# Kernel optimization log

Hardware: AMD Instinct MI355X
Metric: run time of the kernel (lower is better)

The kernel has to match this reference:

```python
import jax, jax.numpy as jnp
import numpy as np

# Dimensions (match input_specs / init_kwargs)
B, T, M, H, E, K = 4, 2048, 1024, 2048, 8, 2
CAP_FACTOR = 1.0  # tutel default capacity_factor
S = B * T
C = int(K * CAP_FACTOR * ((S + E - 1) // E))  # per-expert capacity (tutel Top-k gate)


def setup_inputs() -> dict:
    key = jax.random.key(0)
    ks = jax.random.split(key, 4)
    x = jax.random.normal(ks[0], (B, T, M), jnp.float32)
    wg = jax.random.normal(ks[1], (M, E), jnp.float32) / np.sqrt(M)
    w1 = jax.random.normal(ks[2], (E, M, H), jnp.float32) / np.sqrt(M)
    b1 = jnp.zeros((E, H), jnp.float32)
    w2 = jax.random.normal(ks[3], (E, H, M), jnp.float32) / np.sqrt(H)
    b2 = jnp.zeros((E, M), jnp.float32)
    return {"x": x, "wg": wg, "w1": w1, "b1": b1, "w2": w2, "b2": b2}


def reference(x, wg, w1, b1, w2, b2):
    xf = x.reshape(S, M)
    # ---- Top-k gate (fp32 gate) ----
    logits = xf.astype(jnp.float32) @ wg                 # [S, E]
    scores = jax.nn.softmax(logits, axis=-1)
    topv, topi = jax.lax.top_k(scores, K)                # [S, K]
    gates = topv / (jnp.sum(topv, axis=-1, keepdims=True) + 1e-9)  # normalized top-k gates

    # ---- Dispatch into [E, C, M] buffer with capacity-based token dropping ----
    buf = jnp.zeros((E, C, M), xf.dtype)
    offset = jnp.zeros((E,), jnp.int32)  # tokens already placed per expert (previous slots)
    pos_list, keep_list = [], []
    for j in range(K):  # small fixed loop over top-k slots
        e = topi[:, j]                                   # [S]
        m = jax.nn.one_hot(e, E, dtype=jnp.int32)        # [S, E]
        pos = jnp.sum(jnp.cumsum(m, axis=0) * m, axis=1) - 1 + offset[e]  # position within expert
        offset = offset + jnp.sum(m, axis=0)
        keep = pos < C                                   # drop tokens over capacity
        posc = jnp.minimum(pos, C - 1)
        buf = buf.at[e, posc].add(xf * keep[:, None].astype(xf.dtype))
        pos_list.append(posc)
        keep_list.append(keep)

    # ---- Grouped expert FFN: relu(x W1 + b1) W2 + b2 ----
    h = jax.nn.relu(jnp.einsum('ecm,emh->ech', buf, w1) + b1[:, None, :])  # [E, C, H]
    y = jnp.einsum('ech,ehm->ecm', h, w2) + b2[:, None, :]                 # [E, C, M]

    # ---- Combine with gate weights ----
    out = jnp.zeros_like(xf)
    for j in range(K):
        g = gates[:, j] * keep_list[j].astype(xf.dtype)
        out = out + g[:, None] * y[topi[:, j], pos_list[j]]

    out = out.reshape(B, T, M)
    # result = log_softmax(sum over model_dim, over token dim)
    return jax.nn.log_softmax(jnp.sum(out, axis=2), axis=1)   # [B, T]
```

## Files before the change

### kernel.cpp

```cpp
#include <hip/hip_runtime.h>
#include <hip/hip_bf16.h>
#include <cstdint>
#include <cstddef>

constexpr int Bb = 4;
constexpr int Tt = 2048;
constexpr int Mm = 1024;
constexpr int Hh = 2048;
constexpr int Ee = 8;
constexpr int Ss = Bb * Tt;
constexpr int Cc = 2048;

typedef __attribute__((ext_vector_type(4))) float f32x4;
typedef __attribute__((ext_vector_type(8))) short bf16x8;

__device__ inline void load_lds16(const void* g, void* l) {
    __builtin_amdgcn_global_load_lds(
        (const __attribute__((address_space(1))) unsigned int*)g,
        (__attribute__((address_space(3))) unsigned int*)l, 16, 0, 0);
}

__global__ __launch_bounds__(256) void k_prep(
    const float* __restrict__ w1, const float* __restrict__ w2, const float* __restrict__ b2,
    const float* __restrict__ x, const float* __restrict__ wg,
    __hip_bfloat16* __restrict__ w1t, float* __restrict__ w2sum, float* __restrict__ b2sum,
    int* __restrict__ esel, float* __restrict__ gates, __hip_bfloat16* __restrict__ xbf) {
    int bid = blockIdx.x;
    int t = threadIdx.x;
    if (bid < 4096) {
        __shared__ float tile[64][65];
        int e = bid >> 9, m0 = ((bid >> 5) & 15) * 64, h0 = (bid & 31) * 64;
        const float* src = w1 + (size_t)e * Mm * Hh;
        #pragma unroll
        for (int i = 0; i < 4; i++) {
            int idx = t + i * 256;
            int r = idx >> 4, c4 = idx & 15;
            float4 v = *(const float4*)(src + (size_t)(m0 + r) * Hh + h0 + c4 * 4);
            tile[r][c4 * 4 + 0] = v.x; tile[r][c4 * 4 + 1] = v.y;
            tile[r][c4 * 4 + 2] = v.z; tile[r][c4 * 4 + 3] = v.w;
        }
        __syncthreads();
        __hip_bfloat16* dst = w1t + (size_t)e * Hh * Mm;
        #pragma unroll
        for (int i = 0; i < 2; i++) {
            int idx = t + i * 256;
            int r = idx >> 3, c8 = idx & 7;
            __hip_bfloat16 tmp[8];
            #pragma unroll
            for (int k = 0; k < 8; k++) tmp[k] = __float2bfloat16(tile[c8 * 8 + k][r]);
            uint4 vv; __builtin_memcpy(&vv, tmp, 16);
            *(uint4*)(dst + (size_t)(h0 + r) * Mm + m0 + c8 * 8) = vv;
        }
    } else if (bid < 8192) {
        int wave = t >> 6, lane = t & 63;
        int r = (bid - 4096) * 4 + wave;
        const float4* p = (const float4*)(w2 + (size_t)r * Mm);
        float s = 0.f;
        #pragma unroll
        for (int i = 0; i < 4; i++) { float4 v = p[lane + i * 64]; s += v.x + v.y + v.z + v.w; }
        #pragma unroll
        for (int off = 32; off; off >>= 1) s += __shfl_down(s, off);
        if (lane == 0) w2sum[r] = s;
    } else if (bid == 8192) {
        int wave = t >> 6, lane = t & 63;
        int e = wave * 2 + (lane >> 5);
        int l = lane & 31;
        const float4* p = (const float4*)(b2 + (size_t)e * Mm);
        float s = 0.f;
        #pragma unroll
        for (int i = 0; i < 8; i++) { float4 v = p[l + i * 32]; s += v.x + v.y + v.z + v.w; }
        #pragma unroll
        for (int off = 16; off; off >>= 1) s += __shfl_down(s, off);
        if (l == 0) b2sum[e] = s;
    } else {
        int gb = bid - 8193;
        int s = (gb * 256 + t) >> 6;
        int lane = t & 63;
        const float4* xr = (const float4*)(x + (size_t)s * Mm);
        const float4* wgr = (const float4*)wg;
        float acc[8];
        #pragma unroll
        for (int e = 0; e < 8; e++) acc[e] = 0.f;
        #pragma unroll
        for (int i = 0; i < 4; i++) {
            float4 xv = xr[lane + i * 64];
            __hip_bfloat16 tb[4];
            tb[0] = __float2bfloat16(xv.x); tb[1] = __float2bfloat16(xv.y);
            tb[2] = __float2bfloat16(xv.z); tb[3] = __float2bfloat16(xv.w);
            uint2 u; __builtin_memcpy(&u, tb, 8);
            *(uint2*)(xbf + (size_t)s * Mm + (lane + i * 64) * 4) = u;
            int mbase = (lane + i * 64) * 4;
            #pragma unroll
            for (int k = 0; k < 4; k++) {
                int m = mbase + k;
                float xm = (k == 0) ? xv.x : (k == 1) ? xv.y : (k == 2) ? xv.z : xv.w;
                float4 w0 = wgr[m * 2], w1v = wgr[m * 2 + 1];
                acc[0] += xm * w0.x;  acc[1] += xm * w0.y;  acc[2] += xm * w0.z;  acc[3] += xm * w0.w;
                acc[4] += xm * w1v.x; acc[5] += xm * w1v.y; acc[6] += xm * w1v.z; acc[7] += xm * w1v.w;
            }
        }
        #pragma unroll
        for (int off = 32; off; off >>= 1)
            #pragma unroll
            for (int e = 0; e < 8; e++) acc[e] += __shfl_down(acc[e], off);
        if (lane == 0) {
            float mx = acc[0];
            #pragma unroll
            for (int e = 1; e < 8; e++) mx = fmaxf(mx, acc[e]);
            float p[8], se = 0.f;
            #pragma unroll
            for (int e = 0; e < 8; e++) { p[e] = expf(acc[e] - mx); se += p[e]; }
            float inv = 1.f / se;
            #pragma unroll
            for (int e = 0; e < 8; e++) p[e] *= inv;
            int i0 = 0; float v0 = p[0];
            #pragma unroll
            for (int e = 1; e < 8; e++) if (p[e] > v0) { v0 = p[e]; i0 = e; }
            int i1 = -1; float v1 = -1.f;
            #pragma unroll
            for (int e = 0; e < 8; e++) if (e != i0 && p[e] > v1) { v1 = p[e]; i1 = e; }
            float den = v0 + v1 + 1e-9f;
            esel[s] = i0; esel[Ss + s] = i1;
            gates[s] = v0 / den; gates[Ss + s] = v1 / den;
        }
    }
}

__global__ __launch_bounds__(256) void k_posA(const int* __restrict__ esel,
                                              int* __restrict__ lrank, int* __restrict__ blockhist) {
    int b = blockIdx.x, t = threadIdx.x;
    int d = b * 256 + t;
    int e = esel[d];
    int wave = t >> 6, lane = t & 63;
    __shared__ int wh[4][8];
    unsigned long long mymask = 0;
    #pragma unroll
    for (int q = 0; q < 8; q++) {
        unsigned long long m = __ballot(e == q);
        if (q == e) mymask = m;
        if (lane == 0) wh[wave][q] = (int)__popcll(m);
    }
    __syncthreads();
    int prefix = (int)__popcll(mymask & ((1ull << lane) - 1ull));
    for (int w = 0; w < wave; w++) prefix += wh[w][e];
    lrank[d] = prefix;
    if (t < 8) blockhist[b * 8 + t] = wh[0][t] + wh[1][t] + wh[2][t] + wh[3][t];
}

__global__ void k_posB(const int* __restrict__ blockhist, int* __restrict__ blockbase) {
    int q = threadIdx.x;
    if (q < 8) {
        int run = 0;
        for (int b = 0; b < 64; b++) {
            blockbase[b * 8 + q] = run;
            run += blockhist[b * 8 + q];
        }
    }
}

__global__ __launch_bounds__(256) void k_sidx(const int* __restrict__ esel,
                                              const int* __restrict__ lrank,
                                              const int* __restrict__ blockbase,
                                              int* __restrict__ pos, int* __restrict__ srcidx) {
    int d = blockIdx.x * 256 + threadIdx.x;
    int e = esel[d];
    int p = blockbase[(d >> 8) * 8 + e] + lrank[d];
    pos[d] = p;
    if (p < Cc) srcidx[e * Cc + p] = d & (Ss - 1);
}

__global__ __launch_bounds__(256) void k_gemm(
    const __hip_bfloat16* __restrict__ xbf, const int* __restrict__ srcidx,
    const __hip_bfloat16* __restrict__ w1t,
    const float* __restrict__ b1, const float* __restrict__ w2sum,
    float* __restrict__ rowsum) {
    __shared__ __align__(16) __hip_bfloat16 As[128 * 32];
    __shared__ __align__(16) __hip_bfloat16 Bs[128 * 32];
    int e = blockIdx.y;
    int bid = blockIdx.x;
    int sq = bid >> 4, in16 = bid & 15;
    int hb = (sq & 3) * 4 + (in16 & 3);
    int cb = (sq >> 2) * 4 + (in16 >> 2);
    int c0 = cb * 128, h0 = hb * 128;
    int t = threadIdx.x;
    int wave = t >> 6, lane = t & 63;
    int wm = wave >> 1, wn = wave & 1;
    int r16 = lane & 15, quad = lane >> 4;
    int rq = t >> 2, q = t & 3;
    int s0 = srcidx[e * Cc + c0 + rq];
    int s1 = srcidx[e * Cc + c0 + 64 + rq];
    const __hip_bfloat16* a0 = xbf + (size_t)s0 * Mm + q * 8;
    const __hip_bfloat16* a1 = xbf + (size_t)s1 * Mm + q * 8;
    const __hip_bfloat16* Bp = w1t + (size_t)e * Hh * Mm;
    const __hip_bfloat16* b0 = Bp + (size_t)(h0 + rq) * Mm + q * 8;
    const __hip_bfloat16* b1p = Bp + (size_t)(h0 + 64 + rq) * Mm + q * 8;
    f32x4 acc[4][4];
    #pragma unroll
    for (int i = 0; i < 4; i++)
        #pragma unroll
        for (int j = 0; j < 4; j++) acc[i][j] = (f32x4){0.f, 0.f, 0.f, 0.f};

    for (int k0 = 0; k0 < Mm; k0 += 32) {
        load_lds16(a0 + k0, As + t * 8);
        load_lds16(a1 + k0, As + (256 + t) * 8);
        load_lds16(b0 + k0, Bs + t * 8);
        load_lds16(b1p + k0, Bs + (256 + t) * 8);
        __syncthreads();
        bf16x8 af[4], bfr[4];
        #pragma unroll
        for (int mi = 0; mi < 4; mi++)
            af[mi] = *(const bf16x8*)(As + (wm * 64 + mi * 16 + r16) * 32 + quad * 8);
        #pragma unroll
        for (int ni = 0; ni < 4; ni++)
            bfr[ni] = *(const bf16x8*)(Bs + (wn * 64 + ni * 16 + r16) * 32 + quad * 8);
        #pragma unroll
        for (int mi = 0; mi < 4; mi++)
            #pragma unroll
            for (int ni = 0; ni < 4; ni++)
                acc[mi][ni] = __builtin_amdgcn_mfma_f32_16x16x32_bf16(af[mi], bfr[ni], acc[mi][ni], 0, 0, 0);
        __syncthreads();
    }

    float b1v[4], wsv[4];
    #pragma unroll
    for (int ni = 0; ni < 4; ni++) {
        int hg = h0 + wn * 64 + ni * 16 + r16;
        b1v[ni] = b1[e * Hh + hg];
        wsv[ni] = w2sum[e * Hh + hg];
    }
    #pragma unroll
    for (int mi = 0; mi < 4; mi++) {
        #pragma unroll
        for (int r = 0; r < 4; r++) {
            float val = 0.f;
            #pragma unroll
            for (int ni = 0; ni < 4; ni++) {
                float sv = acc[mi][ni][r] + b1v[ni];
                val += fmaxf(sv, 0.f) * wsv[ni];
            }
            #pragma unroll
            for (int off = 1; off < 16; off <<= 1) val += __shfl_xor(val, off);
            if (r16 == 0) {
                int cg = c0 + wm * 64 + mi * 16 + quad * 4 + r;
                atomicAdd(&rowsum[e * Cc + cg], val);
            }
        }
    }
}

__global__ __launch_bounds__(1024) void k_final(
    const int* __restrict__ esel, const int* __restrict__ pos,
    const float* __restrict__ gates, const float* __restrict__ rowsum,
    const float* __restrict__ b2sum, float* __restrict__ out) {
    int b = blockIdx.x; int t = threadIdx.x;
    __shared__ float red[1024];
    float vv[2];
    #pragma unroll
    for (int i = 0; i < 2; i++) {
        int tok = t + i * 1024;
        int s = b * Tt + tok;
        float acc = 0.f;
        #pragma unroll
        for (int j = 0; j < 2; j++) {
            int d = j * Ss + s;
            int p = pos[d];
            if (p < Cc) {
                int e = esel[d];
                acc += gates[d] * (rowsum[e * Cc + p] + b2sum[e]);
            }
        }
        vv[i] = acc;
    }
    float m = fmaxf(vv[0], vv[1]);
    red[t] = m; __syncthreads();
    for (int st = 512; st; st >>= 1) { if (t < st) red[t] = fmaxf(red[t], red[t + st]); __syncthreads(); }
    float mx = red[0];
    __syncthreads();
    float se = expf(vv[0] - mx) + expf(vv[1] - mx);
    red[t] = se; __syncthreads();
    for (int st = 512; st; st >>= 1) { if (t < st) red[t] += red[t + st]; __syncthreads(); }
    float lse = logf(red[0]);
    #pragma unroll
    for (int i = 0; i < 2; i++) {
        int tok = t + i * 1024;
        out[b * Tt + tok] = vv[i] - mx - lse;
    }
}

extern "C" void kernel_launch(void* const* d_in, const int* in_sizes, int n_in,
                              void* d_out, int out_size, void* d_ws, size_t ws_size,
                              hipStream_t stream) {
    const float* x  = (const float*)d_in[0];
    const float* wg = (const float*)d_in[1];
    const float* w1 = (const float*)d_in[2];
    const float* b1 = (const float*)d_in[3];
    const float* w2 = (const float*)d_in[4];
    const float* b2 = (const float*)d_in[5];
    float* out = (float*)d_out;

    char* ws = (char*)d_ws;
    size_t off = 0;
    auto alloc = [&](size_t bytes) -> void* {
        void* p = ws + off;
        off += (bytes + 255) & ~(size_t)255;
        return p;
    };
    float* rowsum   = (float*)alloc((size_t)Ee * Cc * 4 + (size_t)Ee * Cc * 4);
    int*   srcidx   = (int*)(rowsum + (size_t)Ee * Cc);
    float* w2sum    = (float*)alloc((size_t)Ee * Hh * 4);
    float* b2sum    = (float*)alloc(Ee * 4);
    int*   esel     = (int*)alloc((size_t)2 * Ss * 4);
    int*   lrank    = (int*)alloc((size_t)2 * Ss * 4);
    int*   blockhist= (int*)alloc((size_t)64 * 8 * 4);
    int*   blockbase= (int*)alloc((size_t)64 * 8 * 4);
    int*   pos      = (int*)alloc((size_t)2 * Ss * 4);
    float* gates    = (float*)alloc((size_t)2 * Ss * 4);
    __hip_bfloat16* xbf = (__hip_bfloat16*)alloc((size_t)Ss * Mm * 2);
    __hip_bfloat16* w1t = (__hip_bfloat16*)alloc((size_t)Ee * Hh * Mm * 2);

    hipMemsetAsync(rowsum, 0, (size_t)2 * Ee * Cc * 4, stream);
    k_prep<<<10241, 256, 0, stream>>>(w1, w2, b2, x, wg, w1t, w2sum, b2sum, esel, gates, xbf);
    k_posA<<<64, 256, 0, stream>>>(esel, lrank, blockhist);
    k_posB<<<1, 64, 0, stream>>>(blockhist, blockbase);
    k_sidx<<<64, 256, 0, stream>>>(esel, lrank, blockbase, pos, srcidx);
    k_gemm<<<dim3(16 * 16, Ee), 256, 0, stream>>>(xbf, srcidx, w1t, b1, w2sum, rowsum);
    k_final<<<Bb, 1024, 0, stream>>>(esel, pos, gates, rowsum, b2sum, out);
}
```

Before: 304.9 us.

## Double-buffer GEMM LDS loads, interleave experts in grid, parallelize scan and combine

The expert GEMM now double-buffers its LDS tiles. It issues the next k-slice's global-to-LDS loads before computing on the current one, with explicit vmcnt waits and barriers, so memory latency overlaps with MFMA work. The grid is flattened so consecutive blocks cycle through experts, which changes how work is spread across CUs and caches. The per-expert block-offset scan becomes a wave-parallel shuffle scan, and the final stage splits into a 32-block combine kernel plus a 4-block log-softmax kernel. This adds LDS use and one extra launch, and the hand-placed waitcnt counts must match the number of outstanding loads exactly.

```diff
diff --git a/kernel.cpp b/kernel.cpp
--- a/kernel.cpp
+++ b/kernel.cpp
@@ -147,15 +147,18 @@
     if (t < 8) blockhist[b * 8 + t] = wh[0][t] + wh[1][t] + wh[2][t] + wh[3][t];
 }
 
-__global__ void k_posB(const int* __restrict__ blockhist, int* __restrict__ blockbase) {
-    int q = threadIdx.x;
-    if (q < 8) {
-        int run = 0;
-        for (int b = 0; b < 64; b++) {
-            blockbase[b * 8 + q] = run;
-            run += blockhist[b * 8 + q];
-        }
-    }
+__global__ __launch_bounds__(512) void k_posB(const int* __restrict__ blockhist,
+                                              int* __restrict__ blockbase) {
+    int t = threadIdx.x;
+    int wave = t >> 6, lane = t & 63;
+    int v = blockhist[lane * 8 + wave];
+    int x = v;
+    #pragma unroll
+    for (int off = 1; off < 64; off <<= 1) {
+        int y = __shfl_up(x, off);
+        if (lane >= off) x += y;
+    }
+    blockbase[lane * 8 + wave] = x - v;
 }
 
 __global__ __launch_bounds__(256) void k_sidx(const int* __restrict__ esel,
@@ -174,11 +177,12 @@
     const __hip_bfloat16* __restrict__ w1t,
     const float* __restrict__ b1, const float* __restrict__ w2sum,
     float* __restrict__ rowsum) {
-    __shared__ __align__(16) __hip_bfloat16 As[128 * 32];
-    __shared__ __align__(16) __hip_bfloat16 Bs[128 * 32];
-    int e = blockIdx.y;
+    __shared__ __align__(16) __hip_bfloat16 As[2][128 * 32];
+    __shared__ __align__(16) __hip_bfloat16 Bs[2][128 * 32];
     int bid = blockIdx.x;
-    int sq = bid >> 4, in16 = bid & 15;
+    int e = bid & 7;
+    int tile = bid >> 3;
+    int sq = tile >> 4, in16 = tile & 15;
     int hb = (sq & 3) * 4 + (in16 & 3);
     int cb = (sq >> 2) * 4 + (in16 >> 2);
     int c0 = cb * 128, h0 = hb * 128;
@@ -200,25 +204,41 @@
         #pragma unroll
         for (int j = 0; j < 4; j++) acc[i][j] = (f32x4){0.f, 0.f, 0.f, 0.f};
 
-    for (int k0 = 0; k0 < Mm; k0 += 32) {
-        load_lds16(a0 + k0, As + t * 8);
-        load_lds16(a1 + k0, As + (256 + t) * 8);
-        load_lds16(b0 + k0, Bs + t * 8);
-        load_lds16(b1p + k0, Bs + (256 + t) * 8);
-        __syncthreads();
+    load_lds16(a0,  As[0] + t * 8);
+    load_lds16(a1,  As[0] + (256 + t) * 8);
+    load_lds16(b0,  Bs[0] + t * 8);
+    load_lds16(b1p, Bs[0] + (256 + t) * 8);
+
+    #pragma unroll 2
+    for (int tt = 0; tt < 32; ++tt) {
+        int cur = tt & 1;
+        __builtin_amdgcn_sched_barrier(0);
+        if (tt < 31) {
+            int k0 = (tt + 1) * 32;
+            load_lds16(a0 + k0,  As[cur ^ 1] + t * 8);
+            load_lds16(a1 + k0,  As[cur ^ 1] + (256 + t) * 8);
+            load_lds16(b0 + k0,  Bs[cur ^ 1] + t * 8);
+            load_lds16(b1p + k0, Bs[cur ^ 1] + (256 + t) * 8);
+            asm volatile("s_waitcnt vmcnt(4)" ::: "memory");
+        } else {
+            asm volatile("s_waitcnt vmcnt(0)" ::: "memory");
+        }
+        __builtin_amdgcn_s_barrier();
+        __builtin_amdgcn_sched_barrier(0);
         bf16x8 af[4], bfr[4];
         #pragma unroll
         for (int mi = 0; mi < 4; mi++)
-            af[mi] = *(const bf16x8*)(As + (wm * 64 + mi * 16 + r16) * 32 + quad * 8);
+            af[mi] = *(const bf16x8*)(As[cur] + (wm * 64 + mi * 16 + r16) * 32 + quad * 8);
         #pragma unroll
         for (int ni = 0; ni < 4; ni++)
-            bfr[ni] = *(const bf16x8*)(Bs + (wn * 64 + ni * 16 + r16) * 32 + quad * 8);
+            bfr[ni] = *(const bf16x8*)(Bs[cur] + (wn * 64 + ni * 16 + r16) * 32 + quad * 8);
         #pragma unroll
         for (int mi = 0; mi < 4; mi++)
             #pragma unroll
             for (int ni = 0; ni < 4; ni++)
                 acc[mi][ni] = __builtin_amdgcn_mfma_f32_16x16x32_bf16(af[mi], bfr[ni], acc[mi][ni], 0, 0, 0);
-        __syncthreads();
+        __builtin_amdgcn_sched_barrier(0);
+        __builtin_amdgcn_s_barrier();
     }
 
     float b1v[4], wsv[4];
@@ -248,43 +268,41 @@
     }
 }
 
-__global__ __launch_bounds__(1024) void k_final(
+__global__ __launch_bounds__(256) void k_combine(
     const int* __restrict__ esel, const int* __restrict__ pos,
     const float* __restrict__ gates, const float* __restrict__ rowsum,
-    const float* __restrict__ b2sum, float* __restrict__ out) {
+    const float* __restrict__ b2sum, float* __restrict__ vals) {
+    int s = blockIdx.x * 256 + threadIdx.x;
+    float acc = 0.f;
+    #pragma unroll
+    for (int j = 0; j < 2; j++) {
+        int d = j * Ss + s;
+        int p = pos[d];
+        if (p < Cc) {
+            int ee = esel[d];
+            acc += gates[d] * (rowsum[ee * Cc + p] + b2sum[ee]);
+        }
+    }
+    vals[s] = acc;
+}
+
+__global__ __launch_bounds__(1024) void k_lsm(const float* __restrict__ vals,
+                                              float* __restrict__ out) {
     int b = blockIdx.x; int t = threadIdx.x;
     __shared__ float red[1024];
-    float vv[2];
-    #pragma unroll
-    for (int i = 0; i < 2; i++) {
-        int tok = t + i * 1024;
-        int s = b * Tt + tok;
-        float acc = 0.f;
-        #pragma unroll
-        for (int j = 0; j < 2; j++) {
-            int d = j * Ss + s;
-            int p = pos[d];
-            if (p < Cc) {
-                int e = esel[d];
-                acc += gates[d] * (rowsum[e * Cc + p] + b2sum[e]);
-            }
-        }
-        vv[i] = acc;
-    }
-    float m = fmaxf(vv[0], vv[1]);
+    float v0 = vals[b * Tt + t];
+    float v1 = vals[b * Tt + t + 1024];
+    float m = fmaxf(v0, v1);
     red[t] = m; __syncthreads();
     for (int st = 512; st; st >>= 1) { if (t < st) red[t] = fmaxf(red[t], red[t + st]); __syncthreads(); }
     float mx = red[0];
     __syncthreads();
-    float se = expf(vv[0] - mx) + expf(vv[1] - mx);
+    float se = expf(v0 - mx) + expf(v1 - mx);
     red[t] = se; __syncthreads();
     for (int st = 512; st; st >>= 1) { if (t < st) red[t] += red[t + st]; __syncthreads(); }
     float lse = logf(red[0]);
-    #pragma unroll
-    for (int i = 0; i < 2; i++) {
-        int tok = t + i * 1024;
-        out[b * Tt + tok] = vv[i] - mx - lse;
-    }
+    out[b * Tt + t] = v0 - mx - lse;
+    out[b * Tt + t + 1024] = v1 - mx - lse;
 }
 
 extern "C" void kernel_launch(void* const* d_in, const int* in_sizes, int n_in,
@@ -321,8 +339,10 @@
     hipMemsetAsync(rowsum, 0, (size_t)2 * Ee * Cc * 4, stream);
     k_prep<<<10241, 256, 0, stream>>>(w1, w2, b2, x, wg, w1t, w2sum, b2sum, esel, gates, xbf);
     k_posA<<<64, 256, 0, stream>>>(esel, lrank, blockhist);
-    k_posB<<<1, 64, 0, stream>>>(blockhist, blockbase);
+    k_posB<<<1, 512, 0, stream>>>(blockhist, blockbase);
     k_sidx<<<64, 256, 0, stream>>>(esel, lrank, blockbase, pos, srcidx);
-    k_gemm<<<dim3(16 * 16, Ee), 256, 0, stream>>>(xbf, srcidx, w1t, b1, w2sum, rowsum);
-    k_final<<<Bb, 1024, 0, stream>>>(esel, pos, gates, rowsum, b2sum, out);
-}
+    k_gemm<<<2048, 256, 0, stream>>>(xbf, srcidx, w1t, b1, w2sum, rowsum);
+    float* vals = (float*)lrank;
+    k_combine<<<32, 256, 0, stream>>>(esel, pos, gates, rowsum, b2sum, vals);
+    k_lsm<<<Bb, 1024, 0, stream>>>(vals, out);
+}
```

Measured after the change: 309.6 us. No clear change (+1.5%).
